# Kernel optimization log

Measured on AMD Instinct MI355X. Metric: run time of the kernel, lower is better.

Reference implementation:

```python
import jax, jax.numpy as jnp
import numpy as np

N, E, NG = 50000, 800000, 256          # nodes, edges, graphs
NODE, EDGE, HID, OUT = 64, 16, 64, 1   # feature dims
NUM_LAYERS = 3


def _lin(key, fan_in, fan_out):
    # torch Linear default init: U(-1/sqrt(fan_in), 1/sqrt(fan_in))
    kw, kb = jax.random.split(key)
    bound = 1.0 / np.sqrt(fan_in)
    W = jax.random.uniform(kw, (fan_in, fan_out), jnp.float32, -bound, bound)
    b = jax.random.uniform(kb, (fan_out,), jnp.float32, -bound, bound)
    return W, b


def setup_inputs() -> dict:
    key = jax.random.key(0)
    ks = jax.random.split(key, 8)
    x = jax.random.normal(ks[0], (N, NODE), jnp.float32)
    edge_attr = jax.random.normal(ks[1], (E, EDGE), jnp.float32)
    edge_index = jax.random.randint(ks[2], (2, E), 0, N, dtype=jnp.int32)
    batch = jnp.sort(jax.random.randint(ks[3], (N,), 0, NG, dtype=jnp.int32))
    W_nh, b_nh = _lin(ks[4], NODE, HID)                 # node_to_hidden
    W_mh, b_mh = _lin(ks[5], 2 * HID + EDGE, HID)       # message_to_hidden
    W_om, b_om = _lin(ks[6], 2 * HID + NODE, HID)       # outMsgLin
    W_out, b_out = _lin(ks[7], HID, OUT)                # outLin
    return {"x": x, "edge_attr": edge_attr,
            "W_nh": W_nh, "b_nh": b_nh, "W_mh": W_mh, "b_mh": b_mh,
            "W_om": W_om, "b_om": b_om, "W_out": W_out, "b_out": b_out,
            "edge_index": edge_index, "batch": batch}


def reference(x, edge_attr, W_nh, b_nh, W_mh, b_mh, W_om, b_om, W_out, b_out,
              edge_index, batch):
    # h0 = relu(node_to_hidden(x))
    h0 = jax.nn.relu(x @ W_nh + b_nh)                      # [N, HID]

    # add_self_loops: append N self edges, self-loop edge_attr filled with 1.0
    self_idx = jnp.arange(N, dtype=edge_index.dtype)
    src = jnp.concatenate([edge_index[0], self_idx])       # x_j index (source)
    dst = jnp.concatenate([edge_index[1], self_idx])       # x_i index (target)
    ea = jnp.concatenate([edge_attr,
                          jnp.ones((N, EDGE), edge_attr.dtype)], axis=0)

    # MPN: num_layers of gather-concat -> scatter-add -> linear + h0 -> relu
    h = h0
    for _ in range(NUM_LAYERS):
        msg = jnp.concatenate([h[dst], h[src], ea], axis=1)        # [E+N, 2H+EDGE]
        agg = jax.ops.segment_sum(msg, dst, num_segments=N)        # [N, 2H+EDGE]
        h = jax.nn.relu(agg @ W_mh + b_mh + h0)                    # [N, HID]

    # outMsg: message = concat[h_i, h_j, x_j], aggr add, update identity
    out_msg = jnp.concatenate([h[dst], h[src], x[src]], axis=1)    # [E+N, 2H+NODE]
    agg2 = jax.ops.segment_sum(out_msg, dst, num_segments=N)       # [N, 2H+NODE]

    out = jax.nn.relu(agg2 @ W_om + b_om)                          # [N, HID]
    pooled = jax.ops.segment_sum(out, batch, num_segments=NG)      # [NG, HID]
    return pooled @ W_out + b_out                                  # [NG, OUT]
```

## Files before the change

### kernel.cpp

```cpp
#include <hip/hip_runtime.h>
#include <hip/hip_fp16.h>

#define N_NODES 50000
#define N_EDGES 800000
#define NGRAPH  256
#define FDIM    64
#define EDIM    16
#define NT      (N_NODES / 16)
#define SH      8
#define M8      (N_NODES * SH)
#define NB8     ((M8 + 255) / 256)
#define CH8     ((NB8 + 255) / 256)
#define NBG     ((N_NODES + 31) / 32)

#define GRPS       8
#define GRP_BLOCKS 256
#define GRID_CF    (GRPS * GRP_BLOCKS)
#define NPG        ((N_NODES + GRPS - 1) / GRPS)

using half8  = __attribute__((ext_vector_type(8))) _Float16;
using float4v = __attribute__((ext_vector_type(4))) float;

__device__ __forceinline__ unsigned hadd2u(unsigned a, unsigned b) {
    __half2 r = __hadd2(__builtin_bit_cast(__half2, a), __builtin_bit_cast(__half2, b));
    return __builtin_bit_cast(unsigned, r);
}
__device__ __forceinline__ unsigned hmul2u(unsigned a, __half2 m) {
    __half2 r = __hmul2(__builtin_bit_cast(__half2, a), m);
    return __builtin_bit_cast(unsigned, r);
}


__global__ __launch_bounds__(256) void k_count(const int* __restrict__ dst,
                                               int* __restrict__ cnt8) {
    int grp = blockIdx.x & (GRPS - 1);
    int bi  = blockIdx.x >> 3;
    int lo = grp * NPG;
    int hi = lo + NPG; if (hi > N_NODES) hi = N_NODES;
    for (int e = bi * 256 + threadIdx.x; e < N_EDGES; e += GRP_BLOCKS * 256) {
        int d = dst[e];
        if (d >= lo && d < hi) atomicAdd(&cnt8[d * SH + (e & (SH - 1))], 1);
    }
}

__global__ void k_cvt_x(const float* __restrict__ x, __half* __restrict__ x16) {
    int t = blockIdx.x * blockDim.x + threadIdx.x;
    if (t < N_NODES * FDIM) x16[t] = __float2half(x[t]);
}

__global__ void k_blksum(const int* __restrict__ cnt8, int* __restrict__ blksum) {
    __shared__ int red[4];
    int b = blockIdx.x, t = threadIdx.x;
    int idx = b * 256 + t;
    int s = (idx < M8) ? cnt8[idx] : 0;
#pragma unroll
    for (int off = 32; off > 0; off >>= 1) s += __shfl_down(s, off, 64);
    int lane = t & 63, wid = t >> 6;
    if (lane == 0) red[wid] = s;
    __syncthreads();
    if (t == 0) blksum[b] = red[0] + red[1] + red[2] + red[3];
}

__global__ void k_scanblk(const int* __restrict__ blksum, int* __restrict__ boff,
                          int* __restrict__ rowp8) {
    __shared__ int sh[256];
    int t = threadIdx.x;
    int base = t * CH8;
    int v[CH8];
    int s = 0;
#pragma unroll
    for (int i = 0; i < CH8; i++) {
        int idx = base + i;
        v[i] = (idx < NB8) ? blksum[idx] : 0;
        s += v[i];
    }
    sh[t] = s;
    __syncthreads();
    for (int off = 1; off < 256; off <<= 1) {
        int u = (t >= off) ? sh[t - off] : 0;
        __syncthreads();
        sh[t] += u;
        __syncthreads();
    }
    int run = (t == 0) ? 0 : sh[t - 1];
#pragma unroll
    for (int i = 0; i < CH8; i++) {
        int idx = base + i;
        if (idx < NB8) boff[idx] = run;
        run += v[i];
    }
    if (t == 255) rowp8[M8] = sh[255];
}

__global__ void k_rowp(const int* __restrict__ cnt8, const int* __restrict__ boff,
                       int* __restrict__ rowp8, int* __restrict__ cur8) {
    __shared__ int sh[256];
    int b = blockIdx.x, t = threadIdx.x;
    int idx = b * 256 + t;
    int v = (idx < M8) ? cnt8[idx] : 0;
    sh[t] = v;
    __syncthreads();
    for (int off = 1; off < 256; off <<= 1) {
        int u = (t >= off) ? sh[t - off] : 0;
        __syncthreads();
        sh[t] += u;
        __syncthreads();
    }
    if (idx < M8) {
        int excl = sh[t] - v + boff[b];
        rowp8[idx] = excl;
        cur8[idx]  = excl;
    }
}

__global__ void k_degf(const int* __restrict__ rowp8, float* __restrict__ degf) {
    int i = blockIdx.x * blockDim.x + threadIdx.x;
    if (i < N_NODES) degf[i] = (float)(rowp8[(i + 1) * SH] - rowp8[i * SH] + 1);
}

__global__ __launch_bounds__(256) void k_fill(const int* __restrict__ src,
                                              const int* __restrict__ dst,
                                              int* __restrict__ cur8,
                                              int2* __restrict__ colperm) {
    int grp = blockIdx.x & (GRPS - 1);
    int bi  = blockIdx.x >> 3;
    int lo = grp * NPG;
    int hi = lo + NPG; if (hi > N_NODES) hi = N_NODES;
    for (int e = bi * 256 + threadIdx.x; e < N_EDGES; e += GRP_BLOCKS * 256) {
        int d = dst[e];
        if (d >= lo && d < hi) {
            int pos = atomicAdd(&cur8[d * SH + (e & (SH - 1))], 1);
            colperm[pos] = make_int2(src[e], e);
        }
    }
}


__global__ __launch_bounds__(256, 8) void k_gather(
    const __half* __restrict__ h16,
    const int* __restrict__ rowp8, const int2* __restrict__ colperm,
    __half* __restrict__ agg16) {
    int lane = threadIdx.x & 63, wid = threadIdx.x >> 6;
    int g = lane >> 3;
    int c = lane & 7;
    const uint4* h8 = (const uint4*)h16;
    int node = (blockIdx.x * 4 + wid) * 8 + g;
    if (node >= N_NODES) return;
    int beg = rowp8[node * SH], end = rowp8[(node + 1) * SH];
    float a0 = 0, a1 = 0, a2 = 0, a3 = 0, a4 = 0, a5 = 0, a6 = 0, a7 = 0;
    for (int p = beg; p < end; p += 8) {
        int cidx = p + c; if (cidx > end - 1) cidx = end - 1;
        int vj = colperm[cidx].x;
#pragma unroll
        for (int k = 0; k < 8; k++) {
            int j = __shfl(vj, g * 8 + k, 64);
            if (p + k < end) {
                uint4 v = h8[(size_t)j * 8 + c];
                float2 f0 = __half22float2(__builtin_bit_cast(__half2, v.x));
                float2 f1 = __half22float2(__builtin_bit_cast(__half2, v.y));
                float2 f2 = __half22float2(__builtin_bit_cast(__half2, v.z));
                float2 f3 = __half22float2(__builtin_bit_cast(__half2, v.w));
                a0 += f0.x; a1 += f0.y; a2 += f1.x; a3 += f1.y;
                a4 += f2.x; a5 += f2.y; a6 += f3.x; a7 += f3.y;
            }
        }
    }
    uint4 o;
    o.x = __builtin_bit_cast(unsigned, __floats2half2_rn(a0, a1));
    o.y = __builtin_bit_cast(unsigned, __floats2half2_rn(a2, a3));
    o.z = __builtin_bit_cast(unsigned, __floats2half2_rn(a4, a5));
    o.w = __builtin_bit_cast(unsigned, __floats2half2_rn(a6, a7));
    ((uint4*)agg16)[(size_t)node * 8 + c] = o;
}

__global__ __launch_bounds__(256, 8) void k_ea_agg(
    const float* __restrict__ edge_attr,
    const int* __restrict__ rowp8, const int2* __restrict__ colperm,
    float* __restrict__ ea) {
    int lane = threadIdx.x & 63, wid = threadIdx.x >> 6;
    int g = lane >> 3;
    int c = lane & 7;
    const float2* a2p = (const float2*)edge_attr;
    int node = (blockIdx.x * 4 + wid) * 8 + g;
    if (node >= N_NODES) return;
    int beg = rowp8[node * SH], end = rowp8[(node + 1) * SH];
    float x0 = 0.f, x1 = 0.f;
    for (int p = beg; p < end; p += 8) {
        int cidx = p + c; if (cidx > end - 1) cidx = end - 1;
        int vj = colperm[cidx].y;
#pragma unroll
        for (int k = 0; k < 8; k++) {
            int e = __shfl(vj, g * 8 + k, 64);
            if (p + k < end) {
                float2 v = a2p[(size_t)e * 8 + c];
                x0 += v.x; x1 += v.y;
            }
        }
    }
    ((float2*)ea)[(size_t)node * 8 + c] = make_float2(x0, x1);
}

__global__ void k_h0base(const float* __restrict__ x, const float* __restrict__ ea,
                         const float* __restrict__ Wnh, const float* __restrict__ bnh,
                         const float* __restrict__ Wmh, const float* __restrict__ bmh,
                         __half* __restrict__ h0out16, __half* __restrict__ base16) {
    __shared__ __align__(16) float sx[4][FDIM];
    __shared__ __align__(16) float sea[4][EDIM];
    int lane = threadIdx.x & 63;
    int wid  = threadIdx.x >> 6;
    float wnh[FDIM], w3[EDIM];
#pragma unroll
    for (int m = 0; m < FDIM; m++) wnh[m] = Wnh[m * FDIM + lane];
    float csum = 0.f;
#pragma unroll
    for (int m = 0; m < EDIM; m++) {
        w3[m] = Wmh[(2 * FDIM + m) * FDIM + lane];
        csum += w3[m];
    }
    float bnhk = bnh[lane], bmhk = bmh[lane];
    int gw = blockIdx.x * 4 + wid;
    int nw = gridDim.x * 4;
    for (int i = gw; i < N_NODES; i += nw) {
        sx[wid][lane] = x[i * FDIM + lane];
        if (lane < EDIM) sea[wid][lane] = ea[i * EDIM + lane];
        float acc0 = bnhk, acc1 = 0.f, acc2 = 0.f, acc3 = 0.f;
        const float4* s4 = (const float4*)sx[wid];
#pragma unroll
        for (int m4 = 0; m4 < FDIM / 4; m4++) {
            float4 v = s4[m4];
            acc0 = fmaf(v.x, wnh[4 * m4 + 0], acc0);
            acc1 = fmaf(v.y, wnh[4 * m4 + 1], acc1);
            acc2 = fmaf(v.z, wnh[4 * m4 + 2], acc2);
            acc3 = fmaf(v.w, wnh[4 * m4 + 3], acc3);
        }
        float h0 = fmaxf((acc0 + acc2) + (acc1 + acc3), 0.f);
        float b0 = h0 + bmhk + csum, b1 = 0.f, b2 = 0.f, b3 = 0.f;
        const float4* e4 = (const float4*)sea[wid];
#pragma unroll
        for (int m4 = 0; m4 < EDIM / 4; m4++) {
            float4 v = e4[m4];
            b0 = fmaf(v.x, w3[4 * m4 + 0], b0);
            b1 = fmaf(v.y, w3[4 * m4 + 1], b1);
            b2 = fmaf(v.z, w3[4 * m4 + 2], b2);
            b3 = fmaf(v.w, w3[4 * m4 + 3], b3);
        }
        h0out16[i * FDIM + lane] = __float2half(h0);
        base16[i * FDIM + lane]  = __float2half((b0 + b2) + (b1 + b3));
    }
}

#define SROW 136

__global__ __launch_bounds__(256, 4) void k_mv_mfma(
    const __half* __restrict__ agg16, const __half* __restrict__ hin16,
    const __half* __restrict__ base16, const float* __restrict__ degf,
    const float* __restrict__ Wmh, __half* __restrict__ hout16) {
    __shared__ __align__(16) _Float16 S[4][16 * SROW];
    int lane = threadIdx.x & 63, wid = threadIdx.x >> 6;
    int n = lane & 15, quad = lane >> 4;
    half8 bfr[4][4];
#pragma unroll
    for (int kk = 0; kk < 4; kk++)
#pragma unroll
        for (int nn = 0; nn < 4; nn++) {
            half8 tmp;
#pragma unroll
            for (int j = 0; j < 8; j++) {
                int kp = kk * 32 + quad * 8 + j;
                int krow = (kp < 64) ? (64 + kp) : (kp - 64);
                tmp[j] = (_Float16)Wmh[krow * FDIM + nn * 16 + n];
            }
            bfr[kk][nn] = tmp;
        }
    int t = blockIdx.x * 4 + wid;
    if (t >= NT) return;
    int tb = t * 16;
    {
        int m = lane >> 2, c = lane & 3;
        int node = tb + m;
        const uint4* ag4 = (const uint4*)agg16;
        const uint4* hh4 = (const uint4*)hin16;
        uint4 agA = ag4[(size_t)node * 8 + c * 2];
        uint4 agB = ag4[(size_t)node * 8 + c * 2 + 1];
        uint4 hA  = hh4[(size_t)node * 8 + c * 2];
        uint4 hB  = hh4[(size_t)node * 8 + c * 2 + 1];
        __half dh = __float2half(degf[node]);
        __half2 dh2 = __halves2half2(dh, dh);
        uint4 s2A, s2B, s1A, s1B;
        s2A.x = hadd2u(agA.x, hA.x); s2A.y = hadd2u(agA.y, hA.y);
        s2A.z = hadd2u(agA.z, hA.z); s2A.w = hadd2u(agA.w, hA.w);
        s2B.x = hadd2u(agB.x, hB.x); s2B.y = hadd2u(agB.y, hB.y);
        s2B.z = hadd2u(agB.z, hB.z); s2B.w = hadd2u(agB.w, hB.w);
        s1A.x = hmul2u(hA.x, dh2); s1A.y = hmul2u(hA.y, dh2);
        s1A.z = hmul2u(hA.z, dh2); s1A.w = hmul2u(hA.w, dh2);
        s1B.x = hmul2u(hB.x, dh2); s1B.y = hmul2u(hB.y, dh2);
        s1B.z = hmul2u(hB.z, dh2); s1B.w = hmul2u(hB.w, dh2);
        uint4* Sw = (uint4*)(&S[wid][m * SROW]);
        Sw[c * 2]     = s2A;
        Sw[c * 2 + 1] = s2B;
        Sw[8 + c * 2]     = s1A;
        Sw[8 + c * 2 + 1] = s1B;
    }
    float4v acc[4];
#pragma unroll
    for (int nn = 0; nn < 4; nn++)
#pragma unroll
        for (int r = 0; r < 4; r++)
            acc[nn][r] = __half2float(base16[(size_t)(tb + quad * 4 + r) * FDIM + nn * 16 + n]);
    const _Float16* Sr = S[wid];
#pragma unroll
    for (int kk = 0; kk < 4; kk++) {
        half8 a = *(const half8*)(Sr + (lane & 15) * SROW + kk * 32 + quad * 8);
#pragma unroll
        for (int nn = 0; nn < 4; nn++)
            acc[nn] = __builtin_amdgcn_mfma_f32_16x16x32_f16(a, bfr[kk][nn], acc[nn], 0, 0, 0);
    }
#pragma unroll
    for (int nn = 0; nn < 4; nn++)
#pragma unroll
        for (int r = 0; r < 4; r++)
            hout16[(size_t)(tb + quad * 4 + r) * FDIM + nn * 16 + n] =
                __float2half(fmaxf(acc[nn][r], 0.f));
}

__global__ __launch_bounds__(256, 4) void k_out_mv_mfma(
    const __half* __restrict__ agg16, const __half* __restrict__ hin16,
    const __half* __restrict__ obase16, const float* __restrict__ degf,
    const float* __restrict__ Wom, const float* __restrict__ Wout,
    float* __restrict__ sc) {
    __shared__ __align__(16) _Float16 S[4][16 * SROW];
    int lane = threadIdx.x & 63, wid = threadIdx.x >> 6;
    int n = lane & 15, quad = lane >> 4;
    half8 bfr[4][4];
#pragma unroll
    for (int kk = 0; kk < 4; kk++)
#pragma unroll
        for (int nn = 0; nn < 4; nn++) {
            half8 tmp;
#pragma unroll
            for (int j = 0; j < 8; j++) {
                int kp = kk * 32 + quad * 8 + j;
                int krow = (kp < 64) ? (64 + kp) : (kp - 64);
                tmp[j] = (_Float16)Wom[krow * FDIM + nn * 16 + n];
            }
            bfr[kk][nn] = tmp;
        }
    float wo0 = Wout[n], wo1 = Wout[16 + n], wo2 = Wout[32 + n], wo3 = Wout[48 + n];
    int t = blockIdx.x * 4 + wid;
    if (t >= NT) return;
    int tb = t * 16;
    {
        int m = lane >> 2, c = lane & 3;
        int node = tb + m;
        const uint4* ag4 = (const uint4*)agg16;
        const uint4* hh4 = (const uint4*)hin16;
        uint4 agA = ag4[(size_t)node * 8 + c * 2];
        uint4 agB = ag4[(size_t)node * 8 + c * 2 + 1];
        uint4 hA  = hh4[(size_t)node * 8 + c * 2];
        uint4 hB  = hh4[(size_t)node * 8 + c * 2 + 1];
        __half dh = __float2half(degf[node]);
        __half2 dh2 = __halves2half2(dh, dh);
        uint4 s2A, s2B, s1A, s1B;
        s2A.x = hadd2u(agA.x, hA.x); s2A.y = hadd2u(agA.y, hA.y);
        s2A.z = hadd2u(agA.z, hA.z); s2A.w = hadd2u(agA.w, hA.w);
        s2B.x = hadd2u(agB.x, hB.x); s2B.y = hadd2u(agB.y, hB.y);
        s2B.z = hadd2u(agB.z, hB.z); s2B.w = hadd2u(agB.w, hB.w);
        s1A.x = hmul2u(hA.x, dh2); s1A.y = hmul2u(hA.y, dh2);
        s1A.z = hmul2u(hA.z, dh2); s1A.w = hmul2u(hA.w, dh2);
        s1B.x = hmul2u(hB.x, dh2); s1B.y = hmul2u(hB.y, dh2);
        s1B.z = hmul2u(hB.z, dh2); s1B.w = hmul2u(hB.w, dh2);
        uint4* Sw = (uint4*)(&S[wid][m * SROW]);
        Sw[c * 2]     = s2A;
        Sw[c * 2 + 1] = s2B;
        Sw[8 + c * 2]     = s1A;
        Sw[8 + c * 2 + 1] = s1B;
    }
    float4v acc[4];
#pragma unroll
    for (int nn = 0; nn < 4; nn++)
#pragma unroll
        for (int r = 0; r < 4; r++)
            acc[nn][r] = __half2float(obase16[(size_t)(tb + quad * 4 + r) * FDIM + nn * 16 + n]);
    const _Float16* Sr = S[wid];
#pragma unroll
    for (int kk = 0; kk < 4; kk++) {
        half8 a = *(const half8*)(Sr + (lane & 15) * SROW + kk * 32 + quad * 8);
#pragma unroll
        for (int nn = 0; nn < 4; nn++)
            acc[nn] = __builtin_amdgcn_mfma_f32_16x16x32_f16(a, bfr[kk][nn], acc[nn], 0, 0, 0);
    }
#pragma unroll
    for (int r = 0; r < 4; r++) {
        float s = fmaxf(acc[0][r], 0.f) * wo0 + fmaxf(acc[1][r], 0.f) * wo1
                + fmaxf(acc[2][r], 0.f) * wo2 + fmaxf(acc[3][r], 0.f) * wo3;
        s += __shfl_xor(s, 1, 64);
        s += __shfl_xor(s, 2, 64);
        s += __shfl_xor(s, 4, 64);
        s += __shfl_xor(s, 8, 64);
        if (n == 0) sc[tb + quad * 4 + r] = s;
    }
}

#define SROW2 72
__global__ __launch_bounds__(256, 4) void k_obase_mfma(
    const __half* __restrict__ aggX16, const __half* __restrict__ x16,
    const float* __restrict__ Wom, const float* __restrict__ bom,
    __half* __restrict__ obase16) {
    __shared__ __align__(16) _Float16 S[4][16 * SROW2];
    int lane = threadIdx.x & 63, wid = threadIdx.x >> 6;
    int n = lane & 15, quad = lane >> 4;
    half8 bfr[2][4];
#pragma unroll
    for (int kk = 0; kk < 2; kk++)
#pragma unroll
        for (int nn = 0; nn < 4; nn++) {
            half8 tmp;
#pragma unroll
            for (int j = 0; j < 8; j++) {
                int kp = kk * 32 + quad * 8 + j;
                tmp[j] = (_Float16)Wom[(128 + kp) * FDIM + nn * 16 + n];
            }
            bfr[kk][nn] = tmp;
        }
    float bom_n[4];
#pragma unroll
    for (int nn = 0; nn < 4; nn++) bom_n[nn] = bom[nn * 16 + n];
    int t = blockIdx.x * 4 + wid;
    if (t >= NT) return;
    int tb = t * 16;
    {
        int m = lane >> 2, c = lane & 3;
        int node = tb + m;
        const uint4* ag4 = (const uint4*)aggX16;
        const uint4* xx4 = (const uint4*)x16;
        uint4 agA = ag4[(size_t)node * 8 + c * 2];
        uint4 agB = ag4[(size_t)node * 8 + c * 2 + 1];
        uint4 xA  = xx4[(size_t)node * 8 + c * 2];
        uint4 xB  = xx4[(size_t)node * 8 + c * 2 + 1];
        uint4 sA, sB;
        sA.x = hadd2u(agA.x, xA.x); sA.y = hadd2u(agA.y, xA.y);
        sA.z = hadd2u(agA.z, xA.z); sA.w = hadd2u(agA.w, xA.w);
        sB.x = hadd2u(agB.x, xB.x); sB.y = hadd2u(agB.y, xB.y);
        sB.z = hadd2u(agB.z, xB.z); sB.w = hadd2u(agB.w, xB.w);
        uint4* Sw = (uint4*)(&S[wid][m * SROW2]);
        Sw[c * 2]     = sA;
        Sw[c * 2 + 1] = sB;
    }
    float4v acc[4];
#pragma unroll
    for (int nn = 0; nn < 4; nn++)
#pragma unroll
        for (int r = 0; r < 4; r++) acc[nn][r] = bom_n[nn];
    const _Float16* Sr = S[wid];
#pragma unroll
    for (int kk = 0; kk < 2; kk++) {
        half8 a = *(const half8*)(Sr + (lane & 15) * SROW2 + kk * 32 + quad * 8);
#pragma unroll
        for (int nn = 0; nn < 4; nn++)
            acc[nn] = __builtin_amdgcn_mfma_f32_16x16x32_f16(a, bfr[kk][nn], acc[nn], 0, 0, 0);
    }
#pragma unroll
    for (int nn = 0; nn < 4; nn++)
#pragma unroll
        for (int r = 0; r < 4; r++)
            obase16[(size_t)(tb + quad * 4 + r) * FDIM + nn * 16 + n] =
                __float2half(acc[nn][r]);
}

__global__ void k_pool(const float* __restrict__ sc, const int* __restrict__ batch,
                       const float* __restrict__ b_out, float* __restrict__ out) {
    __shared__ float red[4];
    int g = blockIdx.x, t = threadIdx.x;
    int lo = 0, hi = N_NODES;
    while (lo < hi) { int mid = (lo + hi) >> 1; if (batch[mid] < g) lo = mid + 1; else hi = mid; }
    int lo2 = lo, hi2 = N_NODES;
    while (lo2 < hi2) { int mid = (lo2 + hi2) >> 1; if (batch[mid] < g + 1) lo2 = mid + 1; else hi2 = mid; }
    float s = 0.f;
    for (int i = lo + t; i < lo2; i += 256) s += sc[i];
#pragma unroll
    for (int off = 32; off > 0; off >>= 1) s += __shfl_down(s, off, 64);
    int lane = t & 63, wid = t >> 6;
    if (lane == 0) red[wid] = s;
    __syncthreads();
    if (t == 0) out[g] = red[0] + red[1] + red[2] + red[3] + b_out[0];
}


extern "C" void kernel_launch(void* const* d_in, const int* in_sizes, int n_in,
                              void* d_out, int out_size, void* d_ws, size_t ws_size,
                              hipStream_t stream) {
    const float* x         = (const float*)d_in[0];
    const float* edge_attr = (const float*)d_in[1];
    const float* Wnh       = (const float*)d_in[2];
    const float* bnh       = (const float*)d_in[3];
    const float* Wmh       = (const float*)d_in[4];
    const float* bmh       = (const float*)d_in[5];
    const float* Wom       = (const float*)d_in[6];
    const float* bom       = (const float*)d_in[7];
    const float* Wout      = (const float*)d_in[8];
    const float* bout      = (const float*)d_in[9];
    const int*   eidx      = (const int*)d_in[10];
    const int*   batch     = (const int*)d_in[11];
    const int*   srcI = eidx;
    const int*   dstI = eidx + N_EDGES;
    float* out = (float*)d_out;
    (void)in_sizes; (void)n_in; (void)out_size;

    char* w = (char*)d_ws;
    size_t off = 0;
    auto take = [&](size_t b) -> void* {
        void* p = w + off;
        off = (off + b + 255) & ~(size_t)255;
        return p;
    };
    float*  ea     = (float*)take((size_t)N_NODES * EDIM * 4);
    int*    cnt8   = (int*)take((size_t)M8 * 4);
    int*    rowp8  = (int*)take((size_t)(M8 + 1) * 4);
    int*    cur8   = (int*)take((size_t)M8 * 4);
    float*  degf   = (float*)take((size_t)N_NODES * 4);
    int2*   colperm= (int2*)take((size_t)N_EDGES * 8);
    float*  sc     = (float*)take((size_t)N_NODES * 4);
    int*    blks   = (int*)take((size_t)NB8 * 4);
    int*    boff   = (int*)take((size_t)NB8 * 4);
    __half* x16    = (__half*)take((size_t)N_NODES * FDIM * 2);
    __half* hA16   = (__half*)take((size_t)N_NODES * FDIM * 2);
    __half* hB16   = (__half*)take((size_t)N_NODES * FDIM * 2);
    __half* agg16  = (__half*)take((size_t)N_NODES * FDIM * 2);
    __half* base16 = (__half*)take((size_t)N_NODES * FDIM * 2);
    __half* obase16= (__half*)take((size_t)N_NODES * FDIM * 2);
    (void)ws_size;

    const int MVG = (NT + 3) / 4;
    const int GBG = (NBG + 0);

    hipMemsetAsync(cnt8, 0, (size_t)M8 * 4, stream);
    k_count<<<GRID_CF, 256, 0, stream>>>(dstI, cnt8);
    k_cvt_x<<<(N_NODES * FDIM + 255) / 256, 256, 0, stream>>>(x, x16);
    k_blksum<<<NB8, 256, 0, stream>>>(cnt8, blks);
    k_scanblk<<<1, 256, 0, stream>>>(blks, boff, rowp8);
    k_rowp<<<NB8, 256, 0, stream>>>(cnt8, boff, rowp8, cur8);
    k_degf<<<(N_NODES + 255) / 256, 256, 0, stream>>>(rowp8, degf);
    k_fill<<<GRID_CF, 256, 0, stream>>>(srcI, dstI, cur8, colperm);

    k_gather<<<GBG, 256, 0, stream>>>(x16, rowp8, colperm, agg16);
    k_obase_mfma<<<MVG, 256, 0, stream>>>(agg16, x16, Wom, bom, obase16);
    k_ea_agg<<<GBG, 256, 0, stream>>>(edge_attr, rowp8, colperm, ea);
    k_h0base<<<2048, 256, 0, stream>>>(x, ea, Wnh, bnh, Wmh, bmh, hA16, base16);

    k_gather<<<GBG, 256, 0, stream>>>(hA16, rowp8, colperm, agg16);
    k_mv_mfma<<<MVG, 256, 0, stream>>>(agg16, hA16, base16, degf, Wmh, hB16);

    k_gather<<<GBG, 256, 0, stream>>>(hB16, rowp8, colperm, agg16);
    k_mv_mfma<<<MVG, 256, 0, stream>>>(agg16, hB16, base16, degf, Wmh, hA16);

    k_gather<<<GBG, 256, 0, stream>>>(hA16, rowp8, colperm, agg16);
    k_mv_mfma<<<MVG, 256, 0, stream>>>(agg16, hA16, base16, degf, Wmh, hB16);

    k_gather<<<GBG, 256, 0, stream>>>(hB16, rowp8, colperm, agg16);
    k_out_mv_mfma<<<MVG, 256, 0, stream>>>(agg16, hB16, obase16, degf, Wom, Wout, sc);
    k_pool<<<NGRAPH, 256, 0, stream>>>(sc, batch, bout, out);
}
```

Measured before the change: 379.9 us.

## Shard CSR buckets by source range, split colperm, fuse x-gather with edge-attr aggregation

Within each destination row, edges are now bucketed by source id range (src>>13) instead of edge index mod 8. Neighbor lists therefore come out roughly sorted by source, which should improve locality of the feature gathers. The int2 colperm array is split into separate source and edge arrays, so the per-layer gathers read only 4 bytes per edge. The first x gather and the edge-attribute aggregation are fused into one kernel that walks the adjacency once. In exchange, k_count reads src as well, and shard counts can become unbalanced, though there are only 7 shards.

Result: faster. 363.7 us (-4.3%).

```diff
diff --git a/kernel.cpp b/kernel.cpp
--- a/kernel.cpp
+++ b/kernel.cpp
@@ -18,6 +18,8 @@
 #define GRID_CF    (GRPS * GRP_BLOCKS)
 #define NPG        ((N_NODES + GRPS - 1) / GRPS)
 
+#define SRC_SHARD(s) ((s) >> 13)
+
 using half8  = __attribute__((ext_vector_type(8))) _Float16;
 using float4v = __attribute__((ext_vector_type(4))) float;
 
@@ -31,7 +33,8 @@
 }
 
 
-__global__ __launch_bounds__(256) void k_count(const int* __restrict__ dst,
+__global__ __launch_bounds__(256) void k_count(const int* __restrict__ src,
+                                               const int* __restrict__ dst,
                                                int* __restrict__ cnt8) {
     int grp = blockIdx.x & (GRPS - 1);
     int bi  = blockIdx.x >> 3;
@@ -39,7 +42,7 @@
     int hi = lo + NPG; if (hi > N_NODES) hi = N_NODES;
     for (int e = bi * 256 + threadIdx.x; e < N_EDGES; e += GRP_BLOCKS * 256) {
         int d = dst[e];
-        if (d >= lo && d < hi) atomicAdd(&cnt8[d * SH + (e & (SH - 1))], 1);
+        if (d >= lo && d < hi) atomicAdd(&cnt8[d * SH + SRC_SHARD(src[e])], 1);
     }
 }
 
@@ -121,7 +124,8 @@
 __global__ __launch_bounds__(256) void k_fill(const int* __restrict__ src,
                                               const int* __restrict__ dst,
                                               int* __restrict__ cur8,
-                                              int2* __restrict__ colperm) {
+                                              int* __restrict__ colsrc,
+                                              int* __restrict__ coledge) {
     int grp = blockIdx.x & (GRPS - 1);
     int bi  = blockIdx.x >> 3;
     int lo = grp * NPG;
@@ -129,8 +133,10 @@
     for (int e = bi * 256 + threadIdx.x; e < N_EDGES; e += GRP_BLOCKS * 256) {
         int d = dst[e];
         if (d >= lo && d < hi) {
-            int pos = atomicAdd(&cur8[d * SH + (e & (SH - 1))], 1);
-            colperm[pos] = make_int2(src[e], e);
+            int s = src[e];
+            int pos = atomicAdd(&cur8[d * SH + SRC_SHARD(s)], 1);
+            colsrc[pos]  = s;
+            coledge[pos] = e;
         }
     }
 }
@@ -138,7 +144,7 @@
 
 __global__ __launch_bounds__(256, 8) void k_gather(
     const __half* __restrict__ h16,
-    const int* __restrict__ rowp8, const int2* __restrict__ colperm,
+    const int* __restrict__ rowp8, const int* __restrict__ colsrc,
     __half* __restrict__ agg16) {
     int lane = threadIdx.x & 63, wid = threadIdx.x >> 6;
     int g = lane >> 3;
@@ -150,7 +156,7 @@
     float a0 = 0, a1 = 0, a2 = 0, a3 = 0, a4 = 0, a5 = 0, a6 = 0, a7 = 0;
     for (int p = beg; p < end; p += 8) {
         int cidx = p + c; if (cidx > end - 1) cidx = end - 1;
-        int vj = colperm[cidx].x;
+        int vj = colsrc[cidx];
 #pragma unroll
         for (int k = 0; k < 8; k++) {
             int j = __shfl(vj, g * 8 + k, 64);
@@ -173,30 +179,48 @@
     ((uint4*)agg16)[(size_t)node * 8 + c] = o;
 }
 
-__global__ __launch_bounds__(256, 8) void k_ea_agg(
-    const float* __restrict__ edge_attr,
-    const int* __restrict__ rowp8, const int2* __restrict__ colperm,
-    float* __restrict__ ea) {
+__global__ __launch_bounds__(256, 8) void k_gxea(
+    const __half* __restrict__ h16, const float* __restrict__ edge_attr,
+    const int* __restrict__ rowp8, const int* __restrict__ colsrc,
+    const int* __restrict__ coledge,
+    __half* __restrict__ agg16, float* __restrict__ ea) {
     int lane = threadIdx.x & 63, wid = threadIdx.x >> 6;
     int g = lane >> 3;
     int c = lane & 7;
+    const uint4* h8 = (const uint4*)h16;
     const float2* a2p = (const float2*)edge_attr;
     int node = (blockIdx.x * 4 + wid) * 8 + g;
     if (node >= N_NODES) return;
     int beg = rowp8[node * SH], end = rowp8[(node + 1) * SH];
+    float a0 = 0, a1 = 0, a2 = 0, a3 = 0, a4 = 0, a5 = 0, a6 = 0, a7 = 0;
     float x0 = 0.f, x1 = 0.f;
     for (int p = beg; p < end; p += 8) {
         int cidx = p + c; if (cidx > end - 1) cidx = end - 1;
-        int vj = colperm[cidx].y;
+        int vs = colsrc[cidx];
+        int ve = coledge[cidx];
 #pragma unroll
         for (int k = 0; k < 8; k++) {
-            int e = __shfl(vj, g * 8 + k, 64);
+            int j = __shfl(vs, g * 8 + k, 64);
+            int e = __shfl(ve, g * 8 + k, 64);
             if (p + k < end) {
-                float2 v = a2p[(size_t)e * 8 + c];
-                x0 += v.x; x1 += v.y;
+                uint4 v = h8[(size_t)j * 8 + c];
+                float2 w = a2p[(size_t)e * 8 + c];
+                float2 f0 = __half22float2(__builtin_bit_cast(__half2, v.x));
+                float2 f1 = __half22float2(__builtin_bit_cast(__half2, v.y));
+                float2 f2 = __half22float2(__builtin_bit_cast(__half2, v.z));
+                float2 f3 = __half22float2(__builtin_bit_cast(__half2, v.w));
+                a0 += f0.x; a1 += f0.y; a2 += f1.x; a3 += f1.y;
+                a4 += f2.x; a5 += f2.y; a6 += f3.x; a7 += f3.y;
+                x0 += w.x; x1 += w.y;
             }
         }
     }
+    uint4 o;
+    o.x = __builtin_bit_cast(unsigned, __floats2half2_rn(a0, a1));
+    o.y = __builtin_bit_cast(unsigned, __floats2half2_rn(a2, a3));
+    o.z = __builtin_bit_cast(unsigned, __floats2half2_rn(a4, a5));
+    o.w = __builtin_bit_cast(unsigned, __floats2half2_rn(a6, a7));
+    ((uint4*)agg16)[(size_t)node * 8 + c] = o;
     ((float2*)ea)[(size_t)node * 8 + c] = make_float2(x0, x1);
 }
 
@@ -518,7 +542,8 @@
     int*    rowp8  = (int*)take((size_t)(M8 + 1) * 4);
     int*    cur8   = (int*)take((size_t)M8 * 4);
     float*  degf   = (float*)take((size_t)N_NODES * 4);
-    int2*   colperm= (int2*)take((size_t)N_EDGES * 8);
+    int*    colsrc = (int*)take((size_t)N_EDGES * 4);
+    int*    coledge= (int*)take((size_t)N_EDGES * 4);
     float*  sc     = (float*)take((size_t)N_NODES * 4);
     int*    blks   = (int*)take((size_t)NB8 * 4);
     int*    boff   = (int*)take((size_t)NB8 * 4);
@@ -534,29 +559,29 @@
     const int GBG = (NBG + 0);
 
     hipMemsetAsync(cnt8, 0, (size_t)M8 * 4, stream);
-    k_count<<<GRID_CF, 256, 0, stream>>>(dstI, cnt8);
+    k_count<<<GRID_CF, 256, 0, stream>>>(srcI, dstI, cnt8);
     k_cvt_x<<<(N_NODES * FDIM + 255) / 256, 256, 0, stream>>>(x, x16);
     k_blksum<<<NB8, 256, 0, stream>>>(cnt8, blks);
     k_scanblk<<<1, 256, 0, stream>>>(blks, boff, rowp8);
     k_rowp<<<NB8, 256, 0, stream>>>(cnt8, boff, rowp8, cur8);
     k_degf<<<(N_NODES + 255) / 256, 256, 0, stream>>>(rowp8, degf);
-    k_fill<<<GRID_CF, 256, 0, stream>>>(srcI, dstI, cur8, colperm);
-
-    k_gather<<<GBG, 256, 0, stream>>>(x16, rowp8, colperm, agg16);
+    k_fill<<<GRID_CF, 256, 0, stream>>>(srcI, dstI, cur8, colsrc, coledge);
+
+    k_gxea<<<GBG, 256, 0, stream>>>(x16, edge_attr, rowp8, colsrc, coledge,
+                                    agg16, ea);
     k_obase_mfma<<<MVG, 256, 0, stream>>>(agg16, x16, Wom, bom, obase16);
-    k_ea_agg<<<GBG, 256, 0, stream>>>(edge_attr, rowp8, colperm, ea);
     k_h0base<<<2048, 256, 0, stream>>>(x, ea, Wnh, bnh, Wmh, bmh, hA16, base16);
 
-    k_gather<<<GBG, 256, 0, stream>>>(hA16, rowp8, colperm, agg16);
+    k_gather<<<GBG, 256, 0, stream>>>(hA16, rowp8, colsrc, agg16);
     k_mv_mfma<<<MVG, 256, 0, stream>>>(agg16, hA16, base16, degf, Wmh, hB16);
 
-    k_gather<<<GBG, 256, 0, stream>>>(hB16, rowp8, colperm, agg16);
+    k_gather<<<GBG, 256, 0, stream>>>(hB16, rowp8, colsrc, agg16);
     k_mv_mfma<<<MVG, 256, 0, stream>>>(agg16, hB16, base16, degf, Wmh, hA16);
 
-    k_gather<<<GBG, 256, 0, stream>>>(hA16, rowp8, colperm, agg16);
+    k_gather<<<GBG, 256, 0, stream>>>(hA16, rowp8, colsrc, agg16);
     k_mv_mfma<<<MVG, 256, 0, stream>>>(agg16, hA16, base16, degf, Wmh, hB16);
 
-    k_gather<<<GBG, 256, 0, stream>>>(hB16, rowp8, colperm, agg16);
+    k_gather<<<GBG, 256, 0, stream>>>(hB16, rowp8, colsrc, agg16);
     k_out_mv_mfma<<<MVG, 256, 0, stream>>>(agg16, hB16, obase16, degf, Wom, Wout, sc);
     k_pool<<<NGRAPH, 256, 0, stream>>>(sc, batch, bout, out);
 }
```
